# Kernel tuning notes

Measured on AMD Instinct MI355X. Metric: run time of the kernel, lower is better.

## Reference

```python
import jax, jax.numpy as jnp
import numpy as np

B, T, C, H = 8, 4096, 768, 64  # batch, seq, input_channels, head size


def setup_inputs() -> dict:
    key = jax.random.key(0)
    k1, k2, k3, k4 = jax.random.split(key, 4)
    scale = 1.0 / np.sqrt(C)
    return {
        "x": jax.random.normal(k1, (B, T, C), dtype=jnp.float32),
        "Wk": jax.random.normal(k2, (C, H), dtype=jnp.float32) * scale,
        "Wq": jax.random.normal(k3, (C, H), dtype=jnp.float32) * scale,
        "Wv": jax.random.normal(k4, (C, H), dtype=jnp.float32) * scale,
    }


def reference(x, Wk, Wq, Wv):
    Bc, Tc, Cc = x.shape
    k = x @ Wk  # [B,T,H]
    q = x @ Wq  # [B,T,H]
    v = x @ Wv  # [B,T,H]
    # Note: original scales by C**-0.5 where C = input_channels
    wei = jnp.einsum("bth,bTh->btT", q, k) * (Cc ** -0.5)
    causal = jnp.tril(jnp.ones((Tc, Tc), dtype=bool))
    wei = jnp.where(causal, wei, -jnp.inf)
    wei = jax.nn.softmax(wei, axis=-1)
    # dropout_prob = 0.0 -> identity
    out = jnp.einsum("btT,bTh->bth", wei, v)
    return out
```

## Files before the change

### kernel.cpp

```cpp
#include <hip/hip_runtime.h>

#define TT 4096
#define CCH 768
#define HH 64
#define BBA 8
#define MROWS (BBA*TT)
#define NCHUNK_PB 288

typedef __attribute__((ext_vector_type(8))) short short8;
typedef __attribute__((ext_vector_type(4))) float floatx4;
#if __has_builtin(__builtin_amdgcn_cvt_pk_bf16_f32)
typedef __attribute__((ext_vector_type(2))) __bf16 bf16x2;
#endif

__device__ inline ushort f2bf(float f) {
    union { float f; unsigned u; } v; v.f = f;
    unsigned r = v.u + 0x7fffu + ((v.u >> 16) & 1u);
    return (ushort)(r >> 16);
}

__device__ inline float bf2f(ushort h) {
    union { unsigned u; float f; } v; v.u = ((unsigned)h) << 16;
    return v.f;
}

__device__ inline unsigned pk_bf16(float a, float b) {
#if __has_builtin(__builtin_amdgcn_cvt_pk_bf16_f32)
    union { bf16x2 v; unsigned u; } cv;
    cv.v = __builtin_amdgcn_cvt_pk_bf16_f32(a, b);
    return cv.u;
#else
    union { float f; unsigned u; } x, y; x.f = a; y.f = b;
    unsigned ra = x.u + 0x7fffu + ((x.u >> 16) & 1u);
    unsigned rb = y.u + 0x7fffu + ((y.u >> 16) & 1u);
    return (ra >> 16) | (rb & 0xffff0000u);
#endif
}

__device__ inline float fast_exp2(float x) {
#if __has_builtin(__builtin_amdgcn_exp2f)
    return __builtin_amdgcn_exp2f(x);
#else
    return exp2f(x);
#endif
}

__device__ inline int prm(int r) {
    return (r & ~15) | ((r & 3) << 2) | ((r >> 2) & 3);
}

__global__ __launch_bounds__(256) void wt_kernel(const float* __restrict__ Wq,
                                                 const float* __restrict__ Wk,
                                                 const float* __restrict__ Wv,
                                                 ushort* __restrict__ wt) {
    __shared__ float tile[64][65];
    const int m = blockIdx.x / 12, kt = blockIdx.x % 12;
    const float* W = (m == 0) ? Wq : (m == 1) ? Wk : Wv;
    const int n = threadIdx.x & 63, r0 = threadIdx.x >> 6;
#pragma unroll
    for (int i = 0; i < 16; ++i) {
        int k = r0 * 16 + i;
        tile[k][n] = W[(kt * 64 + k) * 64 + n];
    }
    __syncthreads();
    const int k2 = threadIdx.x & 63, n2 = threadIdx.x >> 6;
#pragma unroll
    for (int i = 0; i < 16; ++i) {
        int nn = n2 * 16 + i;
        wt[(m * 64 + nn) * 768 + kt * 64 + k2] = f2bf(tile[k2][nn]);
    }
}

__global__ __launch_bounds__(256) void proj_kernel(const float* __restrict__ x,
                                                   const ushort* __restrict__ wt,
                                                   ushort* __restrict__ qb,
                                                   ushort* __restrict__ kb,
                                                   ushort* __restrict__ vtg) {
    __shared__ ushort xs[64 * 40];
    __shared__ ushort ws[192 * 40];
    const int tid = threadIdx.x;
    const int w = tid >> 6, lane = tid & 63, c = lane & 15, qd = lane >> 4;
    const int cp = ((c & 3) << 2) | (c >> 2);
    const int rbase = blockIdx.x * 64;
    const int sr = tid >> 2;
    const int psr = prm(sr);
    const int sc = (tid & 3) * 8;

    floatx4 acc[12];
#pragma unroll
    for (int nt = 0; nt < 12; ++nt) acc[nt] = (floatx4){0.f, 0.f, 0.f, 0.f};

    for (int kc = 0; kc < CCH; kc += 32) {
        {
            const float* src = &x[(size_t)(rbase + sr) * CCH + kc + sc];
            float4 f0 = *(const float4*)src;
            float4 f1 = *(const float4*)(src + 4);
            uint4 xv;
            xv.x = pk_bf16(f0.x, f0.y); xv.y = pk_bf16(f0.z, f0.w);
            xv.z = pk_bf16(f1.x, f1.y); xv.w = pk_bf16(f1.z, f1.w);
            *(uint4*)&xs[psr * 40 + sc] = xv;
        }
#pragma unroll
        for (int i = 0; i < 3; ++i) {
            short8 wv = *(const short8*)&wt[(size_t)(i * 64 + sr) * CCH + kc + sc];
            *(short8*)&ws[(i * 64 + psr) * 40 + sc] = wv;
        }
        __syncthreads();
        short8 a = *(const short8*)&xs[(w * 16 + cp) * 40 + qd * 8];
#pragma unroll
        for (int nt = 0; nt < 12; ++nt) {
            short8 bfr = *(const short8*)&ws[(nt * 16 + cp) * 40 + qd * 8];
            acc[nt] = __builtin_amdgcn_mfma_f32_16x16x32_bf16(a, bfr, acc[nt], 0, 0, 0);
        }
        __syncthreads();
    }
#pragma unroll
    for (int nt = 0; nt < 8; ++nt) {
        int ncol = nt * 16 + c;
        ushort* dst = (ncol < 64) ? qb : kb;
        int h = ncol & 63;
#pragma unroll
        for (int r = 0; r < 4; ++r) {
            int rg = rbase + w * 16 + qd * 4 + r;
            dst[(size_t)rg * 64 + h] = f2bf(acc[nt][r]);
        }
    }
    const int bb = rbase >> 12;
    const int tbase = (rbase & 4095) + w * 16 + qd * 4;
#pragma unroll
    for (int nt = 8; nt < 12; ++nt) {
        int h = (nt - 8) * 16 + c;
        uint2 val;
        val.x = pk_bf16(acc[nt][0], acc[nt][1]);
        val.y = pk_bf16(acc[nt][2], acc[nt][3]);
        *(uint2*)&vtg[((size_t)(bb * 64 + h)) * 4096 + tbase] = val;
    }
}

__global__ __launch_bounds__(256) void attn_kernel(const ushort* __restrict__ qb,
                                                   const ushort* __restrict__ kb,
                                                   const ushort* __restrict__ vtg,
                                                   float* __restrict__ out,
                                                   ushort* __restrict__ Opart,
                                                   float* __restrict__ Ol,
                                                   int mode) {
    __shared__ ushort Ks[64 * 72];
    __shared__ ushort Vt[64 * 72];
    __shared__ ushort Pl[4][1024];
    const float scale2 = 0.052058773f;
    const int tid = threadIdx.x;
    const int w = tid >> 6, lane = tid & 63, c = lane & 15, qd = lane >> 4;
    const int bx = blockIdx.x;
    const int b = bx & 7, craw = bx >> 3;

    int qt, chunk, nch, cix;
    if (mode == 0) {
        qt = 63 - craw; nch = 1; chunk = 0; cix = qt;
    } else {
        cix = (NCHUNK_PB - 1) - craw;
        int idx, s;
        if      (cix <   8) { idx = 0; s =   0; }
        else if (cix <  24) { idx = 1; s =   8; }
        else if (cix <  48) { idx = 2; s =  24; }
        else if (cix <  80) { idx = 3; s =  48; }
        else if (cix < 120) { idx = 4; s =  80; }
        else if (cix < 168) { idx = 5; s = 120; }
        else if (cix < 224) { idx = 6; s = 168; }
        else                { idx = 7; s = 224; }
        nch = idx + 1;
        int d = cix - s;
        qt = (idx << 3) + d / nch;
        chunk = d - (d / nch) * nch;
    }
    const int n = qt + 1;
    const int kbeg = chunk * n / nch;
    const int kend = (chunk + 1) * n / nch;
    const bool direct = (nch == 1);
    const int qbase = qt * 64;

    const size_t growq = (size_t)(b * TT + qbase + w * 16 + c);
    short8 qf0 = *(const short8*)&qb[growq * 64 + qd * 8];
    short8 qf1 = *(const short8*)&qb[growq * 64 + 32 + qd * 8];
    floatx4 o[4];
#pragma unroll
    for (int nt = 0; nt < 4; ++nt) o[nt] = (floatx4){0.f, 0.f, 0.f, 0.f};
    float lsum = 0.f;

    const int sr = tid >> 2;
    const int sk = (tid & 3) * 16;
    const int vd = tid >> 2;
    const int vk = (tid & 3) * 16;
    const ushort* kbb = &kb[(size_t)(b * TT) * 64];
    const ushort* vbb = &vtg[(size_t)(b * 64) * 4096];

    short8 k0, k1, v0, v1;
    {
        const ushort* srcK = &kbb[((size_t)(kbeg * 64 + sr)) * 64 + sk];
        k0 = *(const short8*)srcK; k1 = *(const short8*)(srcK + 8);
        const ushort* srcV = &vbb[(size_t)vd * 4096 + kbeg * 64 + vk];
        v0 = *(const short8*)srcV; v1 = *(const short8*)(srcV + 8);
    }

    for (int kt = kbeg; kt < kend; ++kt) {
        __syncthreads();
        *(short8*)&Ks[sr * 72 + sk] = k0;
        *(short8*)&Ks[sr * 72 + sk + 8] = k1;
        *(short8*)&Vt[vd * 72 + vk] = v0;
        *(short8*)&Vt[vd * 72 + vk + 8] = v1;
        __syncthreads();
        if (kt + 1 < kend) {
            const ushort* srcK = &kbb[((size_t)((kt + 1) * 64 + sr)) * 64 + sk];
            k0 = *(const short8*)srcK; k1 = *(const short8*)(srcK + 8);
            const ushort* srcV = &vbb[(size_t)vd * 4096 + (kt + 1) * 64 + vk];
            v0 = *(const short8*)srcV; v1 = *(const short8*)(srcV + 8);
        }
        floatx4 st[4];
#pragma unroll
        for (int mt = 0; mt < 4; ++mt) {
            short8 kf0 = *(const short8*)&Ks[(mt * 16 + c) * 72 + qd * 8];
            short8 kf1 = *(const short8*)&Ks[(mt * 16 + c) * 72 + 32 + qd * 8];
            st[mt] = (floatx4){0.f, 0.f, 0.f, 0.f};
            st[mt] = __builtin_amdgcn_mfma_f32_16x16x32_bf16(kf0, qf0, st[mt], 0, 0, 0);
            st[mt] = __builtin_amdgcn_mfma_f32_16x16x32_bf16(kf1, qf1, st[mt], 0, 0, 0);
        }
        float p[16];
#pragma unroll
        for (int mt = 0; mt < 4; ++mt)
#pragma unroll
            for (int r = 0; r < 4; ++r)
                p[mt * 4 + r] = st[mt][r] * scale2;
        if (kt == qt) {
            const int thr = w * 16 + c;
#pragma unroll
            for (int mt = 0; mt < 4; ++mt)
#pragma unroll
                for (int r = 0; r < 4; ++r) {
                    int kl = mt * 16 + qd * 4 + r;
                    if (kl > thr) p[mt * 4 + r] = -1e30f;
                }
        }
#pragma unroll
        for (int i = 0; i < 16; ++i) { p[i] = fast_exp2(p[i]); lsum += p[i]; }
#pragma unroll
        for (int mt = 0; mt < 4; ++mt) {
            uint2 pk;
            pk.x = pk_bf16(p[mt * 4 + 0], p[mt * 4 + 1]);
            pk.y = pk_bf16(p[mt * 4 + 2], p[mt * 4 + 3]);
            int g = 2 * mt + (qd >> 1);
            int off = c * 64 + ((g ^ (c & 7)) << 3) + ((qd & 1) << 2);
            *(uint2*)&Pl[w][off] = pk;
        }
        short8 pf0 = *(const short8*)&Pl[w][c * 64 + (((qd) ^ (c & 7)) << 3)];
        short8 pf1 = *(const short8*)&Pl[w][c * 64 + (((4 + qd) ^ (c & 7)) << 3)];
#pragma unroll
        for (int nt = 0; nt < 4; ++nt) {
            short8 vf0 = *(const short8*)&Vt[(nt * 16 + c) * 72 + qd * 8];
            short8 vf1 = *(const short8*)&Vt[(nt * 16 + c) * 72 + 32 + qd * 8];
            o[nt] = __builtin_amdgcn_mfma_f32_16x16x32_bf16(pf0, vf0, o[nt], 0, 0, 0);
            o[nt] = __builtin_amdgcn_mfma_f32_16x16x32_bf16(pf1, vf1, o[nt], 0, 0, 0);
        }
    }

    float l_run = lsum;
    l_run += __shfl_xor(l_run, 16);
    l_run += __shfl_xor(l_run, 32);

    if (direct) {
#pragma unroll
        for (int r = 0; r < 4; ++r) {
            float lr = __shfl(l_run, qd * 4 + r);
            float inv = 1.f / lr;
            size_t rowg = (size_t)(b * TT) + qbase + w * 16 + qd * 4 + r;
#pragma unroll
            for (int nt = 0; nt < 4; ++nt)
                out[rowg * 64 + nt * 16 + c] = o[nt][r] * inv;
        }
    } else {
        const int slot = b * NCHUNK_PB + cix;
        ushort* Od = Opart + (size_t)slot * 4096;
#pragma unroll
        for (int r = 0; r < 4; ++r) {
            int row = w * 16 + qd * 4 + r;
#pragma unroll
            for (int nt = 0; nt < 4; ++nt)
                Od[row * 64 + nt * 16 + c] = f2bf(o[nt][r]);
        }
        if (qd == 0)
            Ol[(size_t)slot * 64 + w * 16 + c] = l_run;
    }
}

__global__ __launch_bounds__(256) void combine_kernel(const ushort* __restrict__ Opart,
                                                      const float* __restrict__ Ol,
                                                      float* __restrict__ out) {
    const int b = blockIdx.x & 7;
    const int qt = 8 + (blockIdx.x >> 3);
    const int idx = qt >> 3;
    int s;
    if      (idx == 1) s = 8;
    else if (idx == 2) s = 24;
    else if (idx == 3) s = 48;
    else if (idx == 4) s = 80;
    else if (idx == 5) s = 120;
    else if (idx == 6) s = 168;
    else               s = 224;
    const int nch = idx + 1;
    const int c0 = s + (qt - (idx << 3)) * nch;
    const size_t slot0 = (size_t)(b * NCHUNK_PB + c0);
    const int t = threadIdx.x;
    const int col = t & 63, r0 = t >> 6;

    for (int rr = 0; rr < 16; ++rr) {
        int row = (rr << 2) + r0;
        float S = 0.f, A = 0.f;
        for (int i = 0; i < nch; ++i) {
            S += Ol[(slot0 + i) * 64 + row];
            A += bf2f(Opart[(slot0 + i) * 4096 + row * 64 + col]);
        }
        out[((size_t)(b * TT) + qt * 64 + row) * 64 + col] = A / S;
    }
}

extern "C" void kernel_launch(void* const* d_in, const int* in_sizes, int n_in,
                              void* d_out, int out_size, void* d_ws, size_t ws_size,
                              hipStream_t stream) {
    const float* x  = (const float*)d_in[0];
    const float* Wk = (const float*)d_in[1];
    const float* Wq = (const float*)d_in[2];
    const float* Wv = (const float*)d_in[3];
    float* out = (float*)d_out;

    ushort* qbuf = (ushort*)d_ws;
    ushort* kbuf = qbuf + (size_t)MROWS * 64;
    ushort* vbuf = kbuf + (size_t)MROWS * 64;
    ushort* wt   = vbuf + (size_t)MROWS * 64;
    const size_t base = (size_t)MROWS * 64 * 3 * 2 + (size_t)3 * 64 * CCH * 2;
    ushort* Opart = (ushort*)((char*)d_ws + base);
    float*  Ol    = (float*)((char*)d_ws + base + (size_t)BBA * NCHUNK_PB * 4096 * 2);
    const size_t need = base + (size_t)BBA * NCHUNK_PB * 4096 * 2
                             + (size_t)BBA * NCHUNK_PB * 64 * 4;
    const int split = (ws_size >= need) ? 1 : 0;

    wt_kernel<<<36, 256, 0, stream>>>(Wq, Wk, Wv, wt);
    proj_kernel<<<MROWS / 64, 256, 0, stream>>>(x, wt, qbuf, kbuf, vbuf);
    if (split) {
        attn_kernel<<<BBA * NCHUNK_PB, 256, 0, stream>>>(qbuf, kbuf, vbuf, out, Opart, Ol, 1);
        combine_kernel<<<BBA * 56, 256, 0, stream>>>(Opart, Ol, out);
    } else {
        attn_kernel<<<BBA * 64, 256, 0, stream>>>(qbuf, kbuf, vbuf, out, Opart, Ol, 0);
    }
}
```

Measured before the change: 248.4 us.

## Double K-step to 64 and prefetch next tile into registers in projection

The projection GEMM now processes 64 channels per iteration instead of 32, halving the number of barrier pairs. The next iteration's x and weight data are loaded into registers right after the shared-memory store barrier, so global loads overlap the MFMA work. The row permutation used to avoid LDS bank conflicts is replaced by a plain 72-element padded stride. The trade-off is more registers for the prefetch buffers and possibly different bank-conflict behaviour. This only affects the projection stage, not the attention kernel.

```diff
diff --git a/kernel.cpp b/kernel.cpp
--- a/kernel.cpp
+++ b/kernel.cpp
@@ -45,10 +45,6 @@
 #endif
 }
 
-__device__ inline int prm(int r) {
-    return (r & ~15) | ((r & 3) << 2) | ((r >> 2) & 3);
-}
-
 __global__ __launch_bounds__(256) void wt_kernel(const float* __restrict__ Wq,
                                                  const float* __restrict__ Wk,
                                                  const float* __restrict__ Wv,
@@ -76,41 +72,63 @@
                                                    ushort* __restrict__ qb,
                                                    ushort* __restrict__ kb,
                                                    ushort* __restrict__ vtg) {
-    __shared__ ushort xs[64 * 40];
-    __shared__ ushort ws[192 * 40];
+    __shared__ ushort xs[64 * 72];
+    __shared__ ushort ws[192 * 72];
     const int tid = threadIdx.x;
     const int w = tid >> 6, lane = tid & 63, c = lane & 15, qd = lane >> 4;
-    const int cp = ((c & 3) << 2) | (c >> 2);
     const int rbase = blockIdx.x * 64;
     const int sr = tid >> 2;
-    const int psr = prm(sr);
-    const int sc = (tid & 3) * 8;
+    const int sq = tid & 3;
 
     floatx4 acc[12];
 #pragma unroll
     for (int nt = 0; nt < 12; ++nt) acc[nt] = (floatx4){0.f, 0.f, 0.f, 0.f};
 
-    for (int kc = 0; kc < CCH; kc += 32) {
-        {
-            const float* src = &x[(size_t)(rbase + sr) * CCH + kc + sc];
-            float4 f0 = *(const float4*)src;
-            float4 f1 = *(const float4*)(src + 4);
-            uint4 xv;
-            xv.x = pk_bf16(f0.x, f0.y); xv.y = pk_bf16(f0.z, f0.w);
-            xv.z = pk_bf16(f1.x, f1.y); xv.w = pk_bf16(f1.z, f1.w);
-            *(uint4*)&xs[psr * 40 + sc] = xv;
-        }
-#pragma unroll
-        for (int i = 0; i < 3; ++i) {
-            short8 wv = *(const short8*)&wt[(size_t)(i * 64 + sr) * CCH + kc + sc];
-            *(short8*)&ws[(i * 64 + psr) * 40 + sc] = wv;
-        }
+    const float*  xsrc = &x[(size_t)(rbase + sr) * CCH + sq * 16];
+    const ushort* wsrc0 = &wt[(size_t)(0 * 64 + sr) * CCH + sq * 16];
+    const ushort* wsrc1 = &wt[(size_t)(1 * 64 + sr) * CCH + sq * 16];
+    const ushort* wsrc2 = &wt[(size_t)(2 * 64 + sr) * CCH + sq * 16];
+
+    float4 xr[4];
+    short8 wr[6];
+    xr[0] = *(const float4*)&xsrc[0];  xr[1] = *(const float4*)&xsrc[4];
+    xr[2] = *(const float4*)&xsrc[8];  xr[3] = *(const float4*)&xsrc[12];
+    wr[0] = *(const short8*)&wsrc0[0]; wr[1] = *(const short8*)&wsrc0[8];
+    wr[2] = *(const short8*)&wsrc1[0]; wr[3] = *(const short8*)&wsrc1[8];
+    wr[4] = *(const short8*)&wsrc2[0]; wr[5] = *(const short8*)&wsrc2[8];
+
+    for (int kc = 0; kc < CCH; kc += 64) {
+        uint4 s0, s1;
+        s0.x = pk_bf16(xr[0].x, xr[0].y); s0.y = pk_bf16(xr[0].z, xr[0].w);
+        s0.z = pk_bf16(xr[1].x, xr[1].y); s0.w = pk_bf16(xr[1].z, xr[1].w);
+        s1.x = pk_bf16(xr[2].x, xr[2].y); s1.y = pk_bf16(xr[2].z, xr[2].w);
+        s1.z = pk_bf16(xr[3].x, xr[3].y); s1.w = pk_bf16(xr[3].z, xr[3].w);
+        *(uint4*)&xs[sr * 72 + sq * 16]     = s0;
+        *(uint4*)&xs[sr * 72 + sq * 16 + 8] = s1;
+        *(short8*)&ws[(0 * 64 + sr) * 72 + sq * 16]     = wr[0];
+        *(short8*)&ws[(0 * 64 + sr) * 72 + sq * 16 + 8] = wr[1];
+        *(short8*)&ws[(1 * 64 + sr) * 72 + sq * 16]     = wr[2];
+        *(short8*)&ws[(1 * 64 + sr) * 72 + sq * 16 + 8] = wr[3];
+        *(short8*)&ws[(2 * 64 + sr) * 72 + sq * 16]     = wr[4];
+        *(short8*)&ws[(2 * 64 + sr) * 72 + sq * 16 + 8] = wr[5];
         __syncthreads();
-        short8 a = *(const short8*)&xs[(w * 16 + cp) * 40 + qd * 8];
+        if (kc + 64 < CCH) {
+            xr[0] = *(const float4*)&xsrc[kc + 64];
+            xr[1] = *(const float4*)&xsrc[kc + 68];
+            xr[2] = *(const float4*)&xsrc[kc + 72];
+            xr[3] = *(const float4*)&xsrc[kc + 76];
+            wr[0] = *(const short8*)&wsrc0[kc + 64]; wr[1] = *(const short8*)&wsrc0[kc + 72];
+            wr[2] = *(const short8*)&wsrc1[kc + 64]; wr[3] = *(const short8*)&wsrc1[kc + 72];
+            wr[4] = *(const short8*)&wsrc2[kc + 64]; wr[5] = *(const short8*)&wsrc2[kc + 72];
+        }
+        short8 a0 = *(const short8*)&xs[(w * 16 + c) * 72 + qd * 8];
+        short8 a1 = *(const short8*)&xs[(w * 16 + c) * 72 + 32 + qd * 8];
 #pragma unroll
         for (int nt = 0; nt < 12; ++nt) {
-            short8 bfr = *(const short8*)&ws[(nt * 16 + cp) * 40 + qd * 8];
-            acc[nt] = __builtin_amdgcn_mfma_f32_16x16x32_bf16(a, bfr, acc[nt], 0, 0, 0);
+            short8 b0 = *(const short8*)&ws[(nt * 16 + c) * 72 + qd * 8];
+            short8 b1 = *(const short8*)&ws[(nt * 16 + c) * 72 + 32 + qd * 8];
+            acc[nt] = __builtin_amdgcn_mfma_f32_16x16x32_bf16(a0, b0, acc[nt], 0, 0, 0);
+            acc[nt] = __builtin_amdgcn_mfma_f32_16x16x32_bf16(a1, b1, acc[nt], 0, 0, 0);
         }
         __syncthreads();
     }
```

New measurement: 236.4 us. 1.05x faster.
